# Performance work log

Measured on AMD Instinct MI355X. Metric: run time of the kernel, lower is better.

Reference implementation:

```python
import jax, jax.numpy as jnp
import numpy as np

HEADS = 16
KEY = 64          # key_size == size_per_head
NEG = 1e10


def setup_inputs() -> dict:
    key = jax.random.key(0)
    k1, k2, k3, k4, k5, k6 = jax.random.split(key, 6)
    B, S, D = 2, 2048, 1024
    scale = 1.0 / np.sqrt(D).astype(np.float32)
    return {
        "q": jax.random.normal(k1, (B, S, D), jnp.float32),
        "k": jax.random.normal(k2, (B, S, D), jnp.float32),
        "v": jax.random.normal(k3, (B, S, D), jnp.float32),
        "Wq": jax.random.normal(k4, (D, HEADS * KEY), jnp.float32) * scale,
        "Wk": jax.random.normal(k5, (D, HEADS * KEY), jnp.float32) * scale,
        "Wv": jax.random.normal(k6, (D, HEADS * KEY), jnp.float32) * scale,
    }


def reference(q, k, v, Wq, Wk, Wv):
    B, Sq, _ = q.shape
    Skv = k.shape[1]
    # projections (no bias), split heads: (B, S, H*Dh) -> (B, H, S, Dh)
    qw = (q @ Wq).reshape(B, Sq, HEADS, KEY).transpose(0, 2, 1, 3)
    kw = (k @ Wk).reshape(B, Skv, HEADS, KEY).transpose(0, 2, 1, 3)
    vw = (v @ Wv).reshape(B, Skv, HEADS, KEY).transpose(0, 2, 1, 3)
    inv_sqrt_d = jnp.asarray(1.0 / np.sqrt(KEY), dtype=qw.dtype)
    a = jnp.einsum("bhqd,bhkd->bhqk", qw, kw) * inv_sqrt_d  # (B,H,Sq,Skv)
    # mask_right=True: causal additive mask a - (1 - tril)*1e10
    causal = jnp.tril(jnp.ones((Sq, Skv), dtype=a.dtype))
    a = a - (1.0 - causal) * jnp.asarray(NEG, dtype=a.dtype)
    a = jax.nn.softmax(a, axis=-1)
    o = jnp.einsum("bhqk,bhkd->bhqd", a, vw)  # (B,H,Sq,Dh)
    o = o.transpose(0, 2, 1, 3).reshape(B, Sq, HEADS * KEY)
    return o
```

## Files before the change

### kernel.cpp

```cpp
#include <hip/hip_runtime.h>
#include <hip/hip_bf16.h>

#define HEADS 16
#define KEY   64
#define BB    2
#define SS    2048
#define DD    1024
#define NCOL  1024

typedef __attribute__((ext_vector_type(8))) short bf16x8;
typedef __attribute__((ext_vector_type(4))) float f32x4;
typedef __attribute__((ext_vector_type(8))) unsigned short u16x8;

typedef const __attribute__((address_space(1))) void* gas_ptr;
typedef __attribute__((address_space(3))) void* las_ptr;

__device__ __forceinline__ void gload_lds16(const void* g, void* l) {
  __builtin_amdgcn_global_load_lds((gas_ptr)g, (las_ptr)l, 16, 0, 0);
}

__device__ __forceinline__ unsigned short f2bf(float f) {
  unsigned u = __builtin_bit_cast(unsigned, f);
  u = (u + 0x7FFFu + ((u >> 16) & 1u)) >> 16;
  return (unsigned short)u;
}

__device__ __forceinline__ float bf2f(unsigned short u) {
  return __builtin_bit_cast(float, (unsigned)u << 16);
}

__device__ __forceinline__ unsigned cvtpk(float lo, float hi) {
  unsigned r;
  asm("v_cvt_pk_bf16_f32 %0, %1, %2" : "=v"(r) : "v"(lo), "v"(hi));
  return r;
}

__device__ __forceinline__ f32x4 mfma_bf16(bf16x8 a, bf16x8 b, f32x4 c) {
  return __builtin_amdgcn_mfma_f32_16x16x32_bf16(a, b, c, 0, 0, 0);
}

__global__ __launch_bounds__(256) void cvt3(const float* __restrict__ q,
                                            const float* __restrict__ k,
                                            const float* __restrict__ v,
                                            unsigned short* __restrict__ qo,
                                            unsigned short* __restrict__ ko,
                                            unsigned short* __restrict__ vo) {
  const float* in = blockIdx.y == 0 ? q : (blockIdx.y == 1 ? k : v);
  unsigned short* out = blockIdx.y == 0 ? qo : (blockIdx.y == 1 ? ko : vo);
  int i = blockIdx.x * blockDim.x + threadIdx.x;
  const float4* p = reinterpret_cast<const float4*>(in) + (size_t)i * 2;
  float4 a = p[0], b = p[1];
  u16x8 o;
  o[0] = f2bf(a.x); o[1] = f2bf(a.y); o[2] = f2bf(a.z); o[3] = f2bf(a.w);
  o[4] = f2bf(b.x); o[5] = f2bf(b.y); o[6] = f2bf(b.z); o[7] = f2bf(b.w);
  reinterpret_cast<u16x8*>(out)[i] = o;
}

__global__ __launch_bounds__(1024) void trw(const float* __restrict__ W0,
                                            const float* __restrict__ W1,
                                            const float* __restrict__ W2,
                                            unsigned short* __restrict__ T0,
                                            unsigned short* __restrict__ T1,
                                            unsigned short* __restrict__ T2) {
  const float* W = blockIdx.z == 0 ? W0 : (blockIdx.z == 1 ? W1 : W2);
  unsigned short* T = blockIdx.z == 0 ? T0 : (blockIdx.z == 1 ? T1 : T2);
  __shared__ float tile[32][33];
  int tx = threadIdx.x, ty = threadIdx.y;
  tile[ty][tx] = W[(size_t)(blockIdx.y * 32 + ty) * DD + blockIdx.x * 32 + tx];
  __syncthreads();
  T[(size_t)(blockIdx.x * 32 + ty) * DD + blockIdx.y * 32 + tx] = f2bf(tile[tx][ty]);
}

__global__ __launch_bounds__(256) void gemm_proj3(
    const unsigned short* __restrict__ X0, const unsigned short* __restrict__ X1,
    const unsigned short* __restrict__ X2,
    const unsigned short* __restrict__ W0, const unsigned short* __restrict__ W1,
    const unsigned short* __restrict__ W2,
    unsigned short* __restrict__ O0, unsigned short* __restrict__ O1,
    unsigned short* __restrict__ O2) {
  const int mode = blockIdx.z;
  const unsigned short* X; const unsigned short* WT; unsigned short* O;
  if (mode == 0)      { X = X0; WT = W0; O = O0; }
  else if (mode == 1) { X = X1; WT = W1; O = O1; }
  else                { X = X2; WT = W2; O = O2; }

  __shared__ __align__(16) unsigned short As[128 * 64];
  __shared__ __align__(16) unsigned short Bs[128 * 64];

  const int tid = threadIdx.x;
  const int w = tid >> 6;
  const int l = tid & 63;
  const int m0 = blockIdx.x * 128, n0 = blockIdx.y * 128;
  const int wm = (w >> 1) * 64, wn = (w & 1) * 64;
  const int g = l >> 4, c = l & 15;

  const int srow = tid >> 3;
  const int scol = 8 * ((tid & 7) ^ ((tid >> 3) & 7));

  f32x4 acc[4][4] = {};

  for (int k0 = 0; k0 < DD; k0 += 64) {
#pragma unroll
    for (int i = 0; i < 4; ++i) {
      gload_lds16(X + (size_t)(m0 + i * 32 + srow) * DD + k0 + scol,
                  (char*)As + i * 4096 + w * 1024);
      gload_lds16(WT + (size_t)(n0 + i * 32 + srow) * DD + k0 + scol,
                  (char*)Bs + i * 4096 + w * 1024);
    }
    __syncthreads();
    bf16x8 af[2][4], bfr[2][4];
#pragma unroll
    for (int kk = 0; kk < 2; kk++) {
      const int kb = (((kk << 2) | g) ^ (c & 7)) << 3;
#pragma unroll
      for (int mi = 0; mi < 4; mi++)
        af[kk][mi] = *reinterpret_cast<const bf16x8*>(&As[(wm + mi * 16 + c) * 64 + kb]);
#pragma unroll
      for (int ni = 0; ni < 4; ni++)
        bfr[kk][ni] = *reinterpret_cast<const bf16x8*>(&Bs[(wn + ni * 16 + c) * 64 + kb]);
    }
    if (mode == 2) {
      __builtin_amdgcn_s_setprio(1);
#pragma unroll
      for (int kk = 0; kk < 2; kk++)
#pragma unroll
        for (int mi = 0; mi < 4; mi++)
#pragma unroll
          for (int ni = 0; ni < 4; ni++)
            acc[mi][ni] = mfma_bf16(bfr[kk][ni], af[kk][mi], acc[mi][ni]);
      __builtin_amdgcn_s_setprio(0);
    } else {
      __builtin_amdgcn_s_setprio(1);
#pragma unroll
      for (int kk = 0; kk < 2; kk++)
#pragma unroll
        for (int mi = 0; mi < 4; mi++)
#pragma unroll
          for (int ni = 0; ni < 4; ni++)
            acc[mi][ni] = mfma_bf16(af[kk][mi], bfr[kk][ni], acc[mi][ni]);
      __builtin_amdgcn_s_setprio(0);
    }
    __syncthreads();
  }

  if (mode != 2) {
    const float osc = (mode == 0) ? 0.180336880f : 1.0f;
#pragma unroll
    for (int mi = 0; mi < 4; mi++)
#pragma unroll
      for (int ni = 0; ni < 4; ni++)
#pragma unroll
        for (int r = 0; r < 4; r++) {
          int row = m0 + wm + mi * 16 + g * 4 + r;
          int col = n0 + wn + ni * 16 + c;
          O[(size_t)row * NCOL + col] = f2bf(acc[mi][ni][r] * osc);
        }
  } else {
#pragma unroll
    for (int mi = 0; mi < 4; mi++) {
      const int mbase = m0 + wm + mi * 16;
      const int bb_ = mbase >> 11;
      const int s = (mbase & 2047) + c;
#pragma unroll
      for (int ni = 0; ni < 4; ni++)
#pragma unroll
        for (int r = 0; r < 4; r++) {
          int n = n0 + wn + ni * 16 + g * 4 + r;
          O[((size_t)(bb_ * 1024 + n) << 11) + s] = f2bf(acc[mi][ni][r]);
        }
    }
  }
}

__global__ __launch_bounds__(256) void attn(const unsigned short* __restrict__ qw,
                                            const unsigned short* __restrict__ kw,
                                            const unsigned short* __restrict__ vt,
                                            unsigned short* __restrict__ opart,
                                            float* __restrict__ mlb,
                                            float* __restrict__ out) {
  __shared__ __align__(16) char smem[40960];
  char* KsRaw = smem;
  char* VsRaw = smem + 16384;
  unsigned short* Pl = (unsigned short*)(smem + 32768);
  float* Osc = (float*)smem;

  const int tid = threadIdx.x, w = tid >> 6, l = tid & 63;
  const int g = l >> 4, c = l & 15;
  const int x = blockIdx.x, h = blockIdx.y, b = blockIdx.z;

  int qt, ci, nchunks;
  if (x < 8)       { qt = x;                ci = 0;            nchunks = 1; }
  else if (x < 24) { qt = 8 + ((x - 8) >> 1);  ci = (x - 8) & 1;  nchunks = 2; }
  else if (x < 48) { qt = 16 + (x - 24) / 3;   ci = (x - 24) % 3; nchunks = 3; }
  else             { qt = 24 + ((x - 48) >> 2); ci = (x - 48) & 3; nchunks = 4; }
  const int nt = qt + 1;
  const int t_begin = ci * 8;
  const int t_end = min(t_begin + 8, nt);
  const int q0 = qt * 64;
  const int cid = (b * HEADS + h) * 80 + x;

  const int qrow = q0 + w * 16 + c;
  const size_t qbase = ((size_t)(b * SS) + qrow) * NCOL + h * KEY;
  bf16x8 qf[2];
  qf[0] = *reinterpret_cast<const bf16x8*>(qw + qbase + g * 8);
  qf[1] = *reinterpret_cast<const bf16x8*>(qw + qbase + g * 8 + 32);

  f32x4 oacc[4] = {};
  float m = -1e30f, lsum = 0.f;

  const int krow = w * 8 + (l >> 3);
  const int kcsw = 8 * ((l & 7) ^ (l >> 3));
  const size_t kbase = (size_t)(b * SS) * NCOL + h * KEY;
  const size_t vbase = (size_t)(b * HEADS + h) * KEY * SS;

  {
    const int kv0 = t_begin * 64;
#pragma unroll
    for (int j = 0; j < 2; ++j) {
      gload_lds16(kw + kbase + (size_t)(kv0 + j * 32 + krow) * NCOL + kcsw,
                  KsRaw + j * 4096 + w * 1024);
      gload_lds16(vt + vbase + (size_t)(j * 32 + krow) * SS + kv0 + kcsw,
                  VsRaw + j * 4096 + w * 1024);
    }
  }
  __syncthreads();

  unsigned short* Pw = Pl + w * 1024;
  int cur = 0;
  for (int it = t_begin; it < t_end; ++it) {
    if (it + 1 < t_end) {
      const int kv1 = (it + 1) * 64, nx = cur ^ 1;
#pragma unroll
      for (int j = 0; j < 2; ++j) {
        gload_lds16(kw + kbase + (size_t)(kv1 + j * 32 + krow) * NCOL + kcsw,
                    KsRaw + nx * 8192 + j * 4096 + w * 1024);
        gload_lds16(vt + vbase + (size_t)(j * 32 + krow) * SS + kv1 + kcsw,
                    VsRaw + nx * 8192 + j * 4096 + w * 1024);
      }
    }
    const unsigned short* Kc = (const unsigned short*)(KsRaw + cur * 8192);
    const unsigned short* Vc = (const unsigned short*)(VsRaw + cur * 8192);

    f32x4 sacc[4] = {};
    __builtin_amdgcn_s_setprio(1);
#pragma unroll
    for (int t = 0; t < 4; t++)
#pragma unroll
      for (int ks = 0; ks < 2; ks++) {
        const int off = ((g | (ks << 2)) ^ (c & 7)) << 3;
        bf16x8 kf = *reinterpret_cast<const bf16x8*>(&Kc[(t * 16 + c) * 64 + off]);
        sacc[t] = mfma_bf16(kf, qf[ks], sacc[t]);
      }
    __builtin_amdgcn_s_setprio(0);

    float p[4][4];
#pragma unroll
    for (int t = 0; t < 4; t++)
#pragma unroll
      for (int r = 0; r < 4; r++) p[t][r] = sacc[t][r];
    if (it == nt - 1) {
#pragma unroll
      for (int t = 0; t < 4; t++)
#pragma unroll
        for (int r = 0; r < 4; r++)
          if (it * 64 + 16 * t + 4 * g + r > qrow) p[t][r] = -3.0e38f;
    }
    float tm[4];
#pragma unroll
    for (int t = 0; t < 4; t++)
      tm[t] = fmaxf(fmaxf(p[t][0], p[t][1]), fmaxf(p[t][2], p[t][3]));
    float pm = fmaxf(fmaxf(tm[0], tm[1]), fmaxf(tm[2], tm[3]));
    pm = fmaxf(pm, __shfl_xor(pm, 16));
    pm = fmaxf(pm, __shfl_xor(pm, 32));
    if (__ballot(pm > m + 8.0f)) {
      float mn = fmaxf(m, pm);
      float al = exp2f(m - mn);
      m = mn; lsum *= al;
#pragma unroll
      for (int t = 0; t < 4; t++) oacc[t] *= al;
    }
    float ts[4];
#pragma unroll
    for (int t = 0; t < 4; t++) {
#pragma unroll
      for (int r = 0; r < 4; r++) p[t][r] = exp2f(p[t][r] - m);
      ts[t] = (p[t][0] + p[t][1]) + (p[t][2] + p[t][3]);
    }
    float rs = (ts[0] + ts[1]) + (ts[2] + ts[3]);
    rs += __shfl_xor(rs, 16);
    rs += __shfl_xor(rs, 32);
    lsum += rs;

#pragma unroll
    for (int t = 0; t < 4; t++)
#pragma unroll
      for (int rr = 0; rr < 2; rr++) {
        unsigned pk = cvtpk(p[t][2 * rr], p[t][2 * rr + 1]);
        int col = 16 * t + 4 * g + 2 * rr;
        *reinterpret_cast<unsigned*>(&Pw[c * 64 + (col ^ ((c & 7) << 3))]) = pk;
      }
    bf16x8 pf[2];
#pragma unroll
    for (int ks = 0; ks < 2; ks++)
      pf[ks] = *reinterpret_cast<const bf16x8*>(
          &Pw[c * 64 + (((g | (ks << 2)) ^ (c & 7)) << 3)]);

    __builtin_amdgcn_s_setprio(1);
#pragma unroll
    for (int t = 0; t < 4; t++)
#pragma unroll
      for (int ks = 0; ks < 2; ks++) {
        const int off = ((g | (ks << 2)) ^ (c & 7)) << 3;
        bf16x8 vf = *reinterpret_cast<const bf16x8*>(&Vc[(t * 16 + c) * 64 + off]);
        oacc[t] = mfma_bf16(vf, pf[ks], oacc[t]);
      }
    __builtin_amdgcn_s_setprio(0);
    __syncthreads();
    cur ^= 1;
  }

  const float inv = (nchunks == 1) ? 1.0f / lsum : 1.0f;
#pragma unroll
  for (int t = 0; t < 4; t++)
#pragma unroll
    for (int rr = 0; rr < 2; rr++) {
      float2 v2 = make_float2(oacc[t][2 * rr] * inv, oacc[t][2 * rr + 1] * inv);
      *reinterpret_cast<float2*>(&Osc[(w * 16 + c) * 72 + 16 * t + 4 * g + 2 * rr]) = v2;
    }
  if (nchunks > 1 && l < 16) {
    float* mlp = mlb + (size_t)cid * 128 + w * 16 + c;
    mlp[0] = m;
    mlp[64] = lsum;
  }
  __syncthreads();

  const int row = tid >> 2, sg = (tid & 3) << 4;
  if (nchunks == 1) {
    float* op = out + ((size_t)(b * SS) + q0 + row) * NCOL + h * KEY + sg;
#pragma unroll
    for (int kk = 0; kk < 4; kk++)
      reinterpret_cast<float4*>(op)[kk] =
          *reinterpret_cast<const float4*>(&Osc[row * 72 + sg + kk * 4]);
  } else {
    unsigned* pp = reinterpret_cast<unsigned*>(opart + (size_t)cid * 4096 + row * 64 + sg);
#pragma unroll
    for (int e = 0; e < 8; e++)
      pp[e] = cvtpk(Osc[row * 72 + sg + 2 * e], Osc[row * 72 + sg + 2 * e + 1]);
  }
}

__global__ __launch_bounds__(256) void attn_reduce(const unsigned short* __restrict__ opart,
                                                   const float* __restrict__ mlb,
                                                   float* __restrict__ out) {
  const int qt = 8 + blockIdx.x, h = blockIdx.y, b = blockIdx.z;
  int base, nc;
  if (qt < 16)      { base = 8 + 2 * (qt - 8);   nc = 2; }
  else if (qt < 24) { base = 24 + 3 * (qt - 16); nc = 3; }
  else              { base = 48 + 4 * (qt - 24); nc = 4; }
  const int cid0 = (b * HEADS + h) * 80 + base;
  const int row = threadIdx.x >> 2, sg = (threadIdx.x & 3) << 4;

  float mv[4], lv[4], M = -1e30f;
#pragma unroll
  for (int i = 0; i < 4; i++)
    if (i < nc) {
      mv[i] = mlb[(size_t)(cid0 + i) * 128 + row];
      lv[i] = mlb[(size_t)(cid0 + i) * 128 + 64 + row];
      M = fmaxf(M, mv[i]);
    }
  float L = 0.f, acc[16];
#pragma unroll
  for (int e = 0; e < 16; e++) acc[e] = 0.f;
#pragma unroll
  for (int i = 0; i < 4; i++)
    if (i < nc) {
      float s = exp2f(mv[i] - M);
      L += s * lv[i];
      const u16x8* pp = reinterpret_cast<const u16x8*>(
          opart + (size_t)(cid0 + i) * 4096 + row * 64 + sg);
      u16x8 o0 = pp[0], o1 = pp[1];
#pragma unroll
      for (int e = 0; e < 8; e++) {
        acc[e]     += s * bf2f(o0[e]);
        acc[8 + e] += s * bf2f(o1[e]);
      }
    }
  const float inv = 1.0f / L;
  float* op = out + ((size_t)(b * SS) + qt * 64 + row) * NCOL + h * KEY + sg;
#pragma unroll
  for (int kk = 0; kk < 4; kk++) {
    float4 v;
    v.x = acc[4 * kk] * inv;     v.y = acc[4 * kk + 1] * inv;
    v.z = acc[4 * kk + 2] * inv; v.w = acc[4 * kk + 3] * inv;
    reinterpret_cast<float4*>(op)[kk] = v;
  }
}

extern "C" void kernel_launch(void* const* d_in, const int* in_sizes, int n_in,
                              void* d_out, int out_size, void* d_ws, size_t ws_size,
                              hipStream_t stream) {
  const float* q  = (const float*)d_in[0];
  const float* k  = (const float*)d_in[1];
  const float* v  = (const float*)d_in[2];
  const float* Wq = (const float*)d_in[3];
  const float* Wk = (const float*)d_in[4];
  const float* Wv = (const float*)d_in[5];
  float* out = (float*)d_out;

  unsigned short* ws  = (unsigned short*)d_ws;
  const size_t ACT = (size_t)4 * 1024 * 1024;
  const size_t WEL = (size_t)1024 * 1024;
  unsigned short* qbf = ws;
  unsigned short* kbf = qbf + ACT;
  unsigned short* vbf = kbf + ACT;
  unsigned short* WqT = vbf + ACT;
  unsigned short* WkT = WqT + WEL;
  unsigned short* WvT = WkT + WEL;
  unsigned short* qwp = WvT + WEL;
  unsigned short* kwp = qwp + ACT;
  unsigned short* vt  = kwp + ACT;
  unsigned short* opart = kbf;
  float*          mlb   = (float*)WvT;

  cvt3<<<dim3(2048, 3), 256, 0, stream>>>(q, k, v, qbf, kbf, vbf);
  trw<<<dim3(32, 32, 3), dim3(32, 32), 0, stream>>>(Wq, Wk, Wv, WqT, WkT, WvT);
  gemm_proj3<<<dim3(32, 8, 3), 256, 0, stream>>>(qbf, kbf, vbf, WqT, WkT, WvT,
                                                 qwp, kwp, vt);
  attn<<<dim3(80, 16, 2), 256, 0, stream>>>(qwp, kwp, vt, opart, mlb, out);
  attn_reduce<<<dim3(24, 16, 2), 256, 0, stream>>>(opart, mlb, out);
}
```

Baseline: 207.4 us.

## Fuse convert/transpose prep kernels and double-buffer projection GEMM LDS tiles

Merges the activation bf16 conversion and weight transpose kernels into one launch, with the transpose using 256-thread blocks that each handle four rows. Restructures the projection GEMM to use K=32 tiles in two LDS buffers, so global-to-LDS loads for the next tile are issued while MFMAs run on the current one, with a new swizzle for the narrower tile. This removes one launch and hides load latency. The cost is twice as many loop iterations, each doing half the MFMA work, plus a changed swizzle pattern.

```diff
diff --git a/kernel.cpp b/kernel.cpp
--- a/kernel.cpp
+++ b/kernel.cpp
@@ -39,36 +39,44 @@
   return __builtin_amdgcn_mfma_f32_16x16x32_bf16(a, b, c, 0, 0, 0);
 }
 
-__global__ __launch_bounds__(256) void cvt3(const float* __restrict__ q,
+__global__ __launch_bounds__(256) void prep(const float* __restrict__ q,
                                             const float* __restrict__ k,
                                             const float* __restrict__ v,
+                                            const float* __restrict__ Wq,
+                                            const float* __restrict__ Wk,
+                                            const float* __restrict__ Wv,
                                             unsigned short* __restrict__ qo,
                                             unsigned short* __restrict__ ko,
-                                            unsigned short* __restrict__ vo) {
-  const float* in = blockIdx.y == 0 ? q : (blockIdx.y == 1 ? k : v);
-  unsigned short* out = blockIdx.y == 0 ? qo : (blockIdx.y == 1 ? ko : vo);
-  int i = blockIdx.x * blockDim.x + threadIdx.x;
-  const float4* p = reinterpret_cast<const float4*>(in) + (size_t)i * 2;
-  float4 a = p[0], b = p[1];
-  u16x8 o;
-  o[0] = f2bf(a.x); o[1] = f2bf(a.y); o[2] = f2bf(a.z); o[3] = f2bf(a.w);
-  o[4] = f2bf(b.x); o[5] = f2bf(b.y); o[6] = f2bf(b.z); o[7] = f2bf(b.w);
-  reinterpret_cast<u16x8*>(out)[i] = o;
-}
-
-__global__ __launch_bounds__(1024) void trw(const float* __restrict__ W0,
-                                            const float* __restrict__ W1,
-                                            const float* __restrict__ W2,
+                                            unsigned short* __restrict__ vo,
                                             unsigned short* __restrict__ T0,
                                             unsigned short* __restrict__ T1,
                                             unsigned short* __restrict__ T2) {
-  const float* W = blockIdx.z == 0 ? W0 : (blockIdx.z == 1 ? W1 : W2);
-  unsigned short* T = blockIdx.z == 0 ? T0 : (blockIdx.z == 1 ? T1 : T2);
-  __shared__ float tile[32][33];
-  int tx = threadIdx.x, ty = threadIdx.y;
-  tile[ty][tx] = W[(size_t)(blockIdx.y * 32 + ty) * DD + blockIdx.x * 32 + tx];
-  __syncthreads();
-  T[(size_t)(blockIdx.x * 32 + ty) * DD + blockIdx.y * 32 + tx] = f2bf(tile[tx][ty]);
+  const int zz = blockIdx.y;
+  __shared__ float t32[32][33];
+  if (blockIdx.x < 2048) {
+    const float* in = zz == 0 ? q : (zz == 1 ? k : v);
+    unsigned short* out = zz == 0 ? qo : (zz == 1 ? ko : vo);
+    int i = blockIdx.x * 256 + threadIdx.x;
+    const float4* p = reinterpret_cast<const float4*>(in) + (size_t)i * 2;
+    float4 a = p[0], b = p[1];
+    u16x8 o;
+    o[0] = f2bf(a.x); o[1] = f2bf(a.y); o[2] = f2bf(a.z); o[3] = f2bf(a.w);
+    o[4] = f2bf(b.x); o[5] = f2bf(b.y); o[6] = f2bf(b.z); o[7] = f2bf(b.w);
+    reinterpret_cast<u16x8*>(out)[i] = o;
+  } else {
+    const float* W = zz == 0 ? Wq : (zz == 1 ? Wk : Wv);
+    unsigned short* T = zz == 0 ? T0 : (zz == 1 ? T1 : T2);
+    const int tile = blockIdx.x - 2048;
+    const int bx = tile & 31, by = tile >> 5;
+    const int tx = threadIdx.x & 31, ty = threadIdx.x >> 5;
+#pragma unroll
+    for (int j = 0; j < 4; j++)
+      t32[ty + 8 * j][tx] = W[(size_t)(by * 32 + ty + 8 * j) * DD + bx * 32 + tx];
+    __syncthreads();
+#pragma unroll
+    for (int j = 0; j < 4; j++)
+      T[(size_t)(bx * 32 + ty + 8 * j) * DD + by * 32 + tx] = f2bf(t32[tx][ty + 8 * j]);
+  }
 }
 
 __global__ __launch_bounds__(256) void gemm_proj3(
@@ -84,64 +92,65 @@
   else if (mode == 1) { X = X1; WT = W1; O = O1; }
   else                { X = X2; WT = W2; O = O2; }
 
-  __shared__ __align__(16) unsigned short As[128 * 64];
-  __shared__ __align__(16) unsigned short Bs[128 * 64];
+  __shared__ __align__(16) unsigned short As[2][128 * 32];
+  __shared__ __align__(16) unsigned short Bs[2][128 * 32];
 
   const int tid = threadIdx.x;
-  const int w = tid >> 6;
-  const int l = tid & 63;
+  const int w = tid >> 6, l = tid & 63;
   const int m0 = blockIdx.x * 128, n0 = blockIdx.y * 128;
   const int wm = (w >> 1) * 64, wn = (w & 1) * 64;
   const int g = l >> 4, c = l & 15;
 
-  const int srow = tid >> 3;
-  const int scol = 8 * ((tid & 7) ^ ((tid >> 3) & 7));
+  const int srow = tid >> 2;
+  const int ssw = (srow & 3) ^ ((srow >> 2) & 3);
+  const int scol = 8 * ((tid & 3) ^ ssw);
+  const int kb = 8 * (g ^ ((c & 3) ^ ((c >> 2) & 3)));
 
   f32x4 acc[4][4] = {};
 
-  for (int k0 = 0; k0 < DD; k0 += 64) {
-#pragma unroll
-    for (int i = 0; i < 4; ++i) {
-      gload_lds16(X + (size_t)(m0 + i * 32 + srow) * DD + k0 + scol,
-                  (char*)As + i * 4096 + w * 1024);
-      gload_lds16(WT + (size_t)(n0 + i * 32 + srow) * DD + k0 + scol,
-                  (char*)Bs + i * 4096 + w * 1024);
-    }
+#define G_STAGE(bsel, k0)                                                        \
+  {                                                                              \
+    _Pragma("unroll")                                                            \
+    for (int i = 0; i < 2; ++i) {                                                \
+      gload_lds16(X + (size_t)(m0 + i * 64 + srow) * DD + (k0) + scol,           \
+                  (char*)As[bsel] + i * 4096 + w * 1024);                        \
+      gload_lds16(WT + (size_t)(n0 + i * 64 + srow) * DD + (k0) + scol,          \
+                  (char*)Bs[bsel] + i * 4096 + w * 1024);                        \
+    }                                                                            \
+  }
+
+  G_STAGE(0, 0);
+  __syncthreads();
+
+  int cur = 0;
+  for (int kt = 0; kt < 32; ++kt) {
+    if (kt < 31) G_STAGE(cur ^ 1, (kt + 1) * 32);
+    bf16x8 af[4], bfr[4];
+#pragma unroll
+    for (int mi = 0; mi < 4; mi++)
+      af[mi] = *reinterpret_cast<const bf16x8*>(&As[cur][(wm + mi * 16 + c) * 32 + kb]);
+#pragma unroll
+    for (int ni = 0; ni < 4; ni++)
+      bfr[ni] = *reinterpret_cast<const bf16x8*>(&Bs[cur][(wn + ni * 16 + c) * 32 + kb]);
+    __builtin_amdgcn_s_setprio(1);
+    if (mode == 2) {
+#pragma unroll
+      for (int mi = 0; mi < 4; mi++)
+#pragma unroll
+        for (int ni = 0; ni < 4; ni++)
+          acc[mi][ni] = mfma_bf16(bfr[ni], af[mi], acc[mi][ni]);
+    } else {
+#pragma unroll
+      for (int mi = 0; mi < 4; mi++)
+#pragma unroll
+        for (int ni = 0; ni < 4; ni++)
+          acc[mi][ni] = mfma_bf16(af[mi], bfr[ni], acc[mi][ni]);
+    }
+    __builtin_amdgcn_s_setprio(0);
     __syncthreads();
-    bf16x8 af[2][4], bfr[2][4];
-#pragma unroll
-    for (int kk = 0; kk < 2; kk++) {
-      const int kb = (((kk << 2) | g) ^ (c & 7)) << 3;
-#pragma unroll
-      for (int mi = 0; mi < 4; mi++)
-        af[kk][mi] = *reinterpret_cast<const bf16x8*>(&As[(wm + mi * 16 + c) * 64 + kb]);
-#pragma unroll
-      for (int ni = 0; ni < 4; ni++)
-        bfr[kk][ni] = *reinterpret_cast<const bf16x8*>(&Bs[(wn + ni * 16 + c) * 64 + kb]);
-    }
-    if (mode == 2) {
-      __builtin_amdgcn_s_setprio(1);
-#pragma unroll
-      for (int kk = 0; kk < 2; kk++)
-#pragma unroll
-        for (int mi = 0; mi < 4; mi++)
-#pragma unroll
-          for (int ni = 0; ni < 4; ni++)
-            acc[mi][ni] = mfma_bf16(bfr[kk][ni], af[kk][mi], acc[mi][ni]);
-      __builtin_amdgcn_s_setprio(0);
-    } else {
-      __builtin_amdgcn_s_setprio(1);
-#pragma unroll
-      for (int kk = 0; kk < 2; kk++)
-#pragma unroll
-        for (int mi = 0; mi < 4; mi++)
-#pragma unroll
-          for (int ni = 0; ni < 4; ni++)
-            acc[mi][ni] = mfma_bf16(af[kk][mi], bfr[kk][ni], acc[mi][ni]);
-      __builtin_amdgcn_s_setprio(0);
-    }
-    __syncthreads();
-  }
+    cur ^= 1;
+  }
+#undef G_STAGE
 
   if (mode != 2) {
     const float osc = (mode == 0) ? 0.180336880f : 1.0f;
@@ -422,8 +431,8 @@
   unsigned short* opart = kbf;
   float*          mlb   = (float*)WvT;
 
-  cvt3<<<dim3(2048, 3), 256, 0, stream>>>(q, k, v, qbf, kbf, vbf);
-  trw<<<dim3(32, 32, 3), dim3(32, 32), 0, stream>>>(Wq, Wk, Wv, WqT, WkT, WvT);
+  prep<<<dim3(3072, 3), 256, 0, stream>>>(q, k, v, Wq, Wk, Wv,
+                                          qbf, kbf, vbf, WqT, WkT, WvT);
   gemm_proj3<<<dim3(32, 8, 3), 256, 0, stream>>>(qbf, kbf, vbf, WqT, WkT, WvT,
                                                  qwp, kwp, vt);
   attn<<<dim3(80, 16, 2), 256, 0, stream>>>(qwp, kwp, vt, opart, mlb, out);
```

Measured after the change: 214.7 us. 1.04x slower.
